# Kernel optimization log

Hardware: AMD Instinct MI355X
Metric: run time of the kernel (lower is better)

## Reference

```python
import math
import jax, jax.numpy as jnp
import numpy as np

B, S, D, H, FF, E, V, RH = 8, 256, 512, 8, 2048, 8, 32000, 256
MAX_PATH, MAX_VISITS = 4, 2
NEG = -1e9
DH = D // H


def _make_pe():
    # PositionalEncoding buffer (sin/cos), sliced to seq len S
    pos = np.arange(S, dtype=np.float32)[:, None]
    div = np.exp(np.arange(0, D, 2, dtype=np.float32) * (-math.log(10000.0) / D))
    pe = np.zeros((S, D), dtype=np.float32)
    pe[:, 0::2] = np.sin(pos * div)
    pe[:, 1::2] = np.cos(pos * div)
    return jnp.asarray(pe[None])  # [1,S,D]


def setup_inputs() -> dict:
    key = jax.random.key(0)
    ks = jax.random.split(key, 12)
    s = 0.02
    return dict(
        input_ids=jax.random.randint(ks[0], (B, S), 0, V),
        emb=jax.random.normal(ks[1], (V, D), jnp.float32) * s,
        pe=_make_pe(),
        Wqkv=jax.random.normal(ks[2], (E, 3 * D, D), jnp.float32) * s,
        bqkv=jnp.zeros((E, 3 * D), jnp.float32),
        Wo=jax.random.normal(ks[3], (E, D, D), jnp.float32) * s,
        bo=jnp.zeros((E, D), jnp.float32),
        W1=jax.random.normal(ks[4], (E, FF, D), jnp.float32) * s,
        b1=jnp.zeros((E, FF), jnp.float32),
        W2=jax.random.normal(ks[5], (E, D, FF), jnp.float32) * s,
        b2=jnp.zeros((E, D), jnp.float32),
        ln1_g=jnp.ones((E, D), jnp.float32), ln1_b=jnp.zeros((E, D), jnp.float32),
        ln2_g=jnp.ones((E, D), jnp.float32), ln2_b=jnp.zeros((E, D), jnp.float32),
        tag=jax.random.normal(ks[6], (E, D), jnp.float32) * 0.01,
        r_w1=jax.random.normal(ks[7], (RH, D), jnp.float32) * s,
        r_b1=jnp.zeros((RH,), jnp.float32),
        r_w2=jax.random.normal(ks[8], (E + 1, RH), jnp.float32) * s,
        r_b2=jnp.zeros((E + 1,), jnp.float32),
        lm_w=jax.random.normal(ks[9], (V, D), jnp.float32) * s,
        lm_b=jnp.zeros((V,), jnp.float32),
    )


def _ln(x, g, b):
    # per-sample gathered LayerNorm params g,b: [B,D]; x: [B,S,D]
    mu = x.mean(-1, keepdims=True)
    var = ((x - mu) ** 2).mean(-1, keepdims=True)
    return (x - mu) * jax.lax.rsqrt(var + 1e-5) * g[:, None, :] + b[:, None, :]


def _expert(x, idx, Wqkv, bqkv, Wo, bo, W1, b1, W2, b2, g1, be1, g2, be2, tag):
    # post-norm TransformerEncoderLayer (eval mode, dropout off) with per-sample expert params
    qkv = jnp.einsum('bsd,bfd->bsf', x, Wqkv[idx]) + bqkv[idx][:, None, :]
    q, k, v = jnp.split(qkv, 3, axis=-1)
    q = q.reshape(B, S, H, DH)
    k = k.reshape(B, S, H, DH)
    v = v.reshape(B, S, H, DH)
    att = jax.nn.softmax(jnp.einsum('bqhd,bkhd->bhqk', q, k) / math.sqrt(DH), axis=-1)
    ctx = jnp.einsum('bhqk,bkhd->bqhd', att, v).reshape(B, S, D)
    attn_out = jnp.einsum('bsd,bod->bso', ctx, Wo[idx]) + bo[idx][:, None, :]
    x = _ln(x + attn_out, g1[idx], be1[idx])
    hid = jax.nn.relu(jnp.einsum('bsd,bfd->bsf', x, W1[idx]) + b1[idx][:, None, :])
    ff = jnp.einsum('bsf,bdf->bsd', hid, W2[idx]) + b2[idx][:, None, :]
    x = _ln(x + ff, g2[idx], be2[idx])
    return x + tag[idx][:, None, :]  # + specialization_tag


def reference(input_ids, emb, pe, Wqkv, bqkv, Wo, bo, W1, b1, W2, b2,
              ln1_g, ln1_b, ln2_g, ln2_b, tag, r_w1, r_b1, r_w2, r_b2, lm_w, lm_b):
    pad_mask = (jnp.arange(V) != 0).astype(emb.dtype)[:, None]  # padding_idx=0 row is zero
    rep = (emb * pad_mask)[input_ids] * math.sqrt(D) + pe[:, :S]
    visits = jnp.zeros((B, E), jnp.int32)
    active = jnp.ones((B,), bool)
    ent_total = jnp.asarray(0.0, rep.dtype)
    for _ in range(MAX_PATH):
        summary = rep.mean(1)  # [B,D]
        h = jax.nn.relu(summary @ r_w1.T + r_b1)
        logits = h @ r_w2.T + r_b2  # [B,E+1], last slot = terminate
        logits = jnp.concatenate(
            [jnp.where(visits >= MAX_VISITS, NEG, logits[:, :E]), logits[:, E:]], axis=1)
        probs = jax.nn.softmax(logits, axis=-1)
        ent = -jnp.sum(probs * jnp.log(probs + 1e-9), axis=-1)
        cnt = jnp.sum(active)
        ent_total = ent_total + jnp.where(
            cnt > 0, jnp.sum(ent * active) / jnp.maximum(cnt, 1).astype(ent.dtype), 0.0)
        choice = jnp.argmax(logits, axis=-1)       # eval mode: hard argmax
        go = active & (choice < E)                 # samples routed to an expert this step
        idx = jnp.where(go, choice, 0)
        visits = visits + jax.nn.one_hot(idx, E, dtype=jnp.int32) * go[:, None].astype(jnp.int32)
        new_rep = _expert(rep, idx, Wqkv, bqkv, Wo, bo, W1, b1, W2, b2,
                          ln1_g, ln1_b, ln2_g, ln2_b, tag)
        rep = jnp.where(go[:, None, None], new_rep, rep)  # terminated/inactive reps frozen
        active = go
    logits_lm = rep @ lm_w.T + lm_b  # [B,S,V]
    return logits_lm, ent_total
```

## Files before the change

kernel.cpp:

```cpp
#include <hip/hip_runtime.h>
#include <hip/hip_bf16.h>

#define NB 8
#define NS 256
#define ND 512
#define NH 8
#define NDH 64
#define NFF 2048
#define NE 8
#define NV 32000
#define NRH 256
#define MAXV 2
#define NEGV (-1e9f)

typedef __attribute__((ext_vector_type(8))) short short8;
typedef __attribute__((ext_vector_type(4))) float f32x4;

__device__ __forceinline__ unsigned short f2bf(float x) {
  unsigned int u = __float_as_uint(x);
  u = (u + 0x7fffu + ((u >> 16) & 1u)) >> 16;
  return (unsigned short)u;
}

__device__ __forceinline__ void gload16(const unsigned short* g, unsigned short* l) {
  __builtin_amdgcn_global_load_lds(
      (const __attribute__((address_space(1))) unsigned int*)g,
      (__attribute__((address_space(3))) unsigned int*)l, 16, 0, 0);
}

__device__ __forceinline__ int swzc(int lane) {
  return (lane & 3) ^ ((lane >> 3) & 3);
}

__device__ __forceinline__ void cast8(const float* s, unsigned short* d, int j) {
  const float4* s4 = (const float4*)s;
  float4 a = s4[j * 2], b = s4[j * 2 + 1];
  short8 v;
  v[0] = (short)f2bf(a.x); v[1] = (short)f2bf(a.y);
  v[2] = (short)f2bf(a.z); v[3] = (short)f2bf(a.w);
  v[4] = (short)f2bf(b.x); v[5] = (short)f2bf(b.y);
  v[6] = (short)f2bf(b.z); v[7] = (short)f2bf(b.w);
  *(short8*)&d[(size_t)j * 8] = v;
}

__global__ __launch_bounds__(256) void k_cast5e(
    const float* s0, unsigned short* d0, int n0,
    const float* s1, unsigned short* d1, int n1,
    const float* s2, unsigned short* d2, int n2,
    const float* s3, unsigned short* d3, int n3,
    const float* s4, unsigned short* d4, int n4,
    int nbcast,
    const int* __restrict__ ids, const float* __restrict__ emb,
    const float* __restrict__ pe, float* __restrict__ rep,
    unsigned short* __restrict__ repb, float* __restrict__ partial,
    int* visits, int* active, float* entp) {
  if (blockIdx.x == 0) {
    if (threadIdx.x < NB * NE) visits[threadIdx.x] = 0;
    if (threadIdx.x < NB) active[threadIdx.x] = 1;
    if (threadIdx.x == 0) *entp = 0.f;
  }
  if ((int)blockIdx.x >= nbcast) {
    int j2 = blockIdx.x - nbcast;
    int rg = j2 & 15, b = j2 >> 4;
    int t = threadIdx.x;
    int c0 = t, c1 = t + 256;
    float p0 = 0.f, p1 = 0.f;
    for (int row = 0; row < 16; ++row) {
      int s = rg * 16 + row;
      int id = ids[b * NS + s];
      float sc = (id != 0) ? 22.627416997969522f : 0.f;
      float v0 = emb[(size_t)id * ND + c0] * sc + pe[(size_t)s * ND + c0];
      float v1 = emb[(size_t)id * ND + c1] * sc + pe[(size_t)s * ND + c1];
      size_t base = ((size_t)b * NS + s) * ND;
      rep[base + c0] = v0; rep[base + c1] = v1;
      repb[base + c0] = f2bf(v0); repb[base + c1] = f2bf(v1);
      p0 += v0; p1 += v1;
    }
    float* pp = partial + ((size_t)b * 16 + rg) * ND;
    pp[c0] = p0; pp[c1] = p1;
    return;
  }
  int j = blockIdx.x * 256 + threadIdx.x;
  if (j < n0) { cast8(s0, d0, j); return; }
  j -= n0;
  if (j < n1) { cast8(s1, d1, j); return; }
  j -= n1;
  if (j < n2) { cast8(s2, d2, j); return; }
  j -= n2;
  if (j < n3) { cast8(s3, d3, j); return; }
  j -= n3;
  if (j < n4) cast8(s4, d4, j);
}

__global__ __launch_bounds__(256) void k_router(const float* __restrict__ partial,
                                                const float* __restrict__ rw1,
                                                const float* __restrict__ rb1,
                                                const float* __restrict__ rw2,
                                                const float* __restrict__ rb2,
                                                int* visits, int* active,
                                                int* idx, int* go, float* ent_total) {
  __shared__ float sm[NB][ND];
  __shared__ float h[NB][NRH];
  __shared__ float lg[NB][NE + 1];
  int t = threadIdx.x;
  for (int i = t; i < NB * ND; i += 256) {
    int bb = i >> 9, d = i & 511;
    const float* pp = partial + ((size_t)bb * 16) * ND + d;
    float s = 0.f;
#pragma unroll
    for (int rg = 0; rg < 16; ++rg) s += pp[(size_t)rg * ND];
    sm[bb][d] = s * (1.f / NS);
  }
  __syncthreads();
  {
    const float* w = rw1 + (size_t)t * ND;
    float acc[NB];
#pragma unroll
    for (int b = 0; b < NB; ++b) acc[b] = rb1[t];
    for (int d = 0; d < ND; ++d) {
      float wv = w[d];
#pragma unroll
      for (int b = 0; b < NB; ++b) acc[b] += sm[b][d] * wv;
    }
#pragma unroll
    for (int b = 0; b < NB; ++b) h[b][t] = fmaxf(acc[b], 0.f);
  }
  __syncthreads();
  if (t < NB * (NE + 1)) {
    int b = t / (NE + 1), e = t % (NE + 1);
    const float* w = rw2 + e * NRH;
    float a = rb2[e];
    for (int r = 0; r < NRH; ++r) a += h[b][r] * w[r];
    lg[b][e] = a;
  }
  __syncthreads();
  if (t == 0) {
    int aprev[NB];
    int cnt = 0;
    for (int b = 0; b < NB; ++b) { aprev[b] = active[b]; cnt += aprev[b]; }
    float entsum = 0.f;
    for (int b = 0; b < NB; ++b) {
      float l[NE + 1];
      for (int e = 0; e < NE; ++e)
        l[e] = (visits[b * NE + e] >= MAXV) ? NEGV : lg[b][e];
      l[NE] = lg[b][NE];
      float m = l[0];
      for (int e = 1; e <= NE; ++e) m = fmaxf(m, l[e]);
      float z = 0.f, p[NE + 1];
      for (int e = 0; e <= NE; ++e) { p[e] = __expf(l[e] - m); z += p[e]; }
      float zi = 1.f / z, ent = 0.f;
      for (int e = 0; e <= NE; ++e) {
        float pp = p[e] * zi;
        ent -= pp * __logf(pp + 1e-9f);
      }
      if (aprev[b]) entsum += ent;
      int ch = 0; float bm = l[0];
      for (int e = 1; e <= NE; ++e) if (l[e] > bm) { bm = l[e]; ch = e; }
      int g = (aprev[b] && ch < NE) ? 1 : 0;
      int ix = g ? ch : 0;
      visits[b * NE + ix] += g;
      idx[b] = ix; go[b] = g; active[b] = g;
    }
    if (cnt > 0) *ent_total += entsum / (float)cnt;
  }
}

template <int OUT, int RELU, int SK>
__global__ __launch_bounds__(256) void k_gemm64p(
    const unsigned short* __restrict__ Aall, int sa,
    const unsigned short* __restrict__ Wall, const float* __restrict__ ball,
    float* __restrict__ Pall, unsigned short* __restrict__ Uall, int so,
    int N, int K,
    unsigned short* __restrict__ Qb, unsigned short* __restrict__ Kb,
    unsigned short* __restrict__ Vt,
    const int* __restrict__ go, const int* __restrict__ idx) {
  int b = blockIdx.z;
  if (!go[b]) return;
  int t = threadIdx.x;
  int lane = t & 63, w = t >> 6;
  int wm = (w >> 1) * 32, wn = (w & 1) * 32;
  int kc = blockIdx.x >> 2;
  int bm = (blockIdx.x & 3) * 64, bn = blockIdx.y * 64;
  int KC = K / SK;
  int lrow = (lane >> 4) * 4, lcol = lane & 15;
  const unsigned short* A = Aall + (size_t)b * sa + kc * KC;
  const unsigned short* W = Wall + (size_t)idx[b] * N * K + kc * KC;

  __shared__ __align__(16) unsigned short As[3][64][32];
  __shared__ __align__(16) unsigned short Bs[3][64][32];
  f32x4 acc[2][2];
#pragma unroll
  for (int i = 0; i < 2; ++i)
#pragma unroll
    for (int j = 0; j < 2; ++j) acc[i][j] = (f32x4){0.f, 0.f, 0.f, 0.f};

  const unsigned short* ga = A + (size_t)(bm + w * 16 + (lane >> 2)) * K + swzc(lane) * 8;
  const unsigned short* gb = W + (size_t)(bn + w * 16 + (lane >> 2)) * K + swzc(lane) * 8;

#define ISSUE64(slot, kt)                        \
  gload16(ga + (kt) * 32, &As[slot][w * 16][0]); \
  gload16(gb + (kt) * 32, &Bs[slot][w * 16][0]);

  int nk = KC >> 5;
  ISSUE64(0, 0)
  ISSUE64(1, 1)
  ISSUE64(2, 2)

  int row0 = lane & 15;
  int cs = ((lane >> 4) ^ ((row0 >> 1) & 3)) * 8;
  for (int it = 0; it < nk; ++it) {
    int rem = nk - 1 - it;
    if (rem >= 2)      asm volatile("s_waitcnt vmcnt(4)" ::: "memory");
    else if (rem == 1) asm volatile("s_waitcnt vmcnt(2)" ::: "memory");
    else               asm volatile("s_waitcnt vmcnt(0)" ::: "memory");
    asm volatile("s_barrier" ::: "memory");
    int sl = it % 3;
    short8 a[2], bfr[2];
#pragma unroll
    for (int mf = 0; mf < 2; ++mf)
      a[mf] = *(const short8*)&As[sl][wm + mf * 16 + row0][cs];
#pragma unroll
    for (int nf = 0; nf < 2; ++nf)
      bfr[nf] = *(const short8*)&Bs[sl][wn + nf * 16 + row0][cs];
#pragma unroll
    for (int mf = 0; mf < 2; ++mf)
#pragma unroll
      for (int nf = 0; nf < 2; ++nf)
        acc[mf][nf] = __builtin_amdgcn_mfma_f32_16x16x32_bf16(a[mf], bfr[nf], acc[mf][nf], 0, 0, 0);
    asm volatile("s_barrier" ::: "memory");
    if (it + 3 < nk) { ISSUE64(sl, it + 3) }
  }
#undef ISSUE64

  if (OUT == 2) {
    const float* bias = ball + (size_t)idx[b] * N;
    int seg = bn >> 9;
#pragma unroll
    for (int nf = 0; nf < 2; ++nf) {
      int col = bn + wn + nf * 16 + lcol;
      float bv = bias[col];
      if (seg < 2) {
        unsigned short* dst = (seg == 0) ? Qb : Kb;
        int cc = col - seg * 512;
#pragma unroll
        for (int mf = 0; mf < 2; ++mf)
#pragma unroll
          for (int r = 0; r < 4; ++r) {
            int row = bm + wm + mf * 16 + lrow + r;
            dst[((size_t)b * NS + row) * ND + cc] = f2bf(acc[mf][nf][r] + bv);
          }
      } else {
        int dcol = col - 1024;
#pragma unroll
        for (int mf = 0; mf < 2; ++mf) {
          int s0 = bm + wm + mf * 16 + lrow;
          unsigned long long pk =
              (unsigned long long)f2bf(acc[mf][nf][0] + bv) |
              ((unsigned long long)f2bf(acc[mf][nf][1] + bv) << 16) |
              ((unsigned long long)f2bf(acc[mf][nf][2] + bv) << 32) |
              ((unsigned long long)f2bf(acc[mf][nf][3] + bv) << 48);
          *(unsigned long long*)&Vt[((size_t)b * 512 + dcol) * 256 + s0] = pk;
        }
      }
    }
  } else if (OUT == 1) {
    const float* bias = ball + (size_t)idx[b] * N;
#pragma unroll
    for (int nf = 0; nf < 2; ++nf) {
      int col = bn + wn + nf * 16 + lcol;
      float bv = bias[col];
#pragma unroll
      for (int mf = 0; mf < 2; ++mf) {
#pragma unroll
        for (int r = 0; r < 4; ++r) {
          int row = bm + wm + mf * 16 + lrow + r;
          float v = acc[mf][nf][r] + bv;
          if (RELU) v = fmaxf(v, 0.f);
          Uall[(size_t)b * so + (size_t)row * N + col] = f2bf(v);
        }
      }
    }
  } else {
    float* P = Pall + ((size_t)kc * NB + b) * ((size_t)NS * N);
#pragma unroll
    for (int nf = 0; nf < 2; ++nf) {
      int col = bn + wn + nf * 16 + lcol;
#pragma unroll
      for (int mf = 0; mf < 2; ++mf)
#pragma unroll
        for (int r = 0; r < 4; ++r)
          P[(size_t)(bm + wm + mf * 16 + lrow + r) * N + col] = acc[mf][nf][r];
    }
  }
}

__global__ __launch_bounds__(256) void k_attn2(const unsigned short* __restrict__ Qb,
                                               const unsigned short* __restrict__ Kb,
                                               const unsigned short* __restrict__ Vt,
                                               unsigned short* __restrict__ ctxb,
                                               const int* __restrict__ go) {
  int b = blockIdx.z, h = blockIdx.y, qt = blockIdx.x;
  if (!go[b]) return;
  int t = threadIdx.x;
  __shared__ __align__(16) unsigned short lds0[16384];
  __shared__ __align__(16) unsigned short lds1[16384];
  int lane = t & 63, w = t >> 6, g = lane >> 4, c = lane & 15;

#pragma unroll
  for (int i = 0; i < 8; ++i) {
    int task = i * 256 + t;
    int k = task >> 3, cc = task & 7;
    short8 v = *(const short8*)&Kb[((size_t)b * NS + k) * ND + h * NDH + cc * 8];
    *(short8*)&lds0[k * 64 + ((cc * 8) ^ ((k & 7) << 3))] = v;
  }
#pragma unroll
  for (int i = 0; i < 8; ++i) {
    int task = i * 256 + t;
    int d = task >> 5, kc = task & 31;
    short8 v = *(const short8*)&Vt[((size_t)b * 512 + h * NDH + d) * 256 + kc * 8];
    *(short8*)&lds1[d * 256 + ((kc * 8) ^ ((d & 7) << 3))] = v;
  }
  short8 qf[2];
  {
    const unsigned short* qp = Qb + ((size_t)b * NS + qt * 64 + w * 16 + c) * ND + h * NDH;
    qf[0] = *(const short8*)&qp[g * 8];
    qf[1] = *(const short8*)&qp[32 + g * 8];
  }
  __syncthreads();

  f32x4 sacc[16];
#pragma unroll
  for (int mf = 0; mf < 16; ++mf) sacc[mf] = (f32x4){0.f, 0.f, 0.f, 0.f};
#pragma unroll
  for (int mf = 0; mf < 16; ++mf) {
#pragma unroll
    for (int kd = 0; kd < 2; ++kd) {
      int row = mf * 16 + c;
      short8 kf = *(const short8*)&lds0[row * 64 + ((kd * 32 + g * 8) ^ ((row & 7) << 3))];
      sacc[mf] = __builtin_amdgcn_mfma_f32_16x16x32_bf16(kf, qf[kd], sacc[mf], 0, 0, 0);
    }
  }
  __syncthreads();

  float mx = -3.4e38f;
#pragma unroll
  for (int mf = 0; mf < 16; ++mf) {
#pragma unroll
    for (int r = 0; r < 4; ++r) {
      sacc[mf][r] *= 0.125f;
      mx = fmaxf(mx, sacc[mf][r]);
    }
  }
  mx = fmaxf(mx, __shfl_xor(mx, 16));
  mx = fmaxf(mx, __shfl_xor(mx, 32));
  float sum = 0.f;
#pragma unroll
  for (int mf = 0; mf < 16; ++mf)
#pragma unroll
    for (int r = 0; r < 4; ++r) {
      float p = __expf(sacc[mf][r] - mx);
      sacc[mf][r] = p;
      sum += p;
    }
  sum += __shfl_xor(sum, 16);
  sum += __shfl_xor(sum, 32);
  float zi = 1.f / sum;

  int q_l = w * 16 + c;
#pragma unroll
  for (int mf = 0; mf < 16; ++mf) {
    unsigned long long pk =
        (unsigned long long)f2bf(sacc[mf][0] * zi) |
        ((unsigned long long)f2bf(sacc[mf][1] * zi) << 16) |
        ((unsigned long long)f2bf(sacc[mf][2] * zi) << 32) |
        ((unsigned long long)f2bf(sacc[mf][3] * zi) << 48);
    *(unsigned long long*)&lds0[q_l * 256 + ((mf * 16 + g * 4) ^ ((q_l & 7) << 3))] = pk;
  }

  f32x4 cacc[4];
#pragma unroll
  for (int nf = 0; nf < 4; ++nf) cacc[nf] = (f32x4){0.f, 0.f, 0.f, 0.f};
#pragma unroll
  for (int ks = 0; ks < 8; ++ks) {
    int prow = w * 16 + c;
    short8 pf = *(const short8*)&lds0[prow * 256 + ((ks * 32 + g * 8) ^ ((prow & 7) << 3))];
#pragma unroll
    for (int nf = 0; nf < 4; ++nf) {
      int vrow = nf * 16 + c;
      short8 vf = *(const short8*)&lds1[vrow * 256 + ((ks * 32 + g * 8) ^ ((vrow & 7) << 3))];
      cacc[nf] = __builtin_amdgcn_mfma_f32_16x16x32_bf16(pf, vf, cacc[nf], 0, 0, 0);
    }
  }
#pragma unroll
  for (int nf = 0; nf < 4; ++nf)
#pragma unroll
    for (int r = 0; r < 4; ++r)
      ctxb[((size_t)b * NS + qt * 64 + w * 16 + g * 4 + r) * ND + h * NDH + nf * 16 + c] =
          f2bf(cacc[nf][r]);
}

template <int NCH, int TAG, int SUMP>
__global__ __launch_bounds__(256) void k_ln_red(
    const float* __restrict__ res, const float* __restrict__ part,
    const float* __restrict__ gbias,
    const float* __restrict__ gall, const float* __restrict__ beall,
    const float* __restrict__ tagall,
    float* __restrict__ outf, unsigned short* __restrict__ outb,
    float* __restrict__ sump,
    const int* __restrict__ go, const int* __restrict__ idx) {
  int b = blockIdx.y;
  if (!go[b]) return;
  int rg = blockIdx.x;
  int w = threadIdx.x >> 6, l = threadIdx.x & 63;
  int ix = idx[b];
  int d = l * 8;
  float gb8[8], gg[8], bb[8];
  {
    float4 a0 = *(const float4*)&gbias[ix * ND + d];
    float4 a1 = *(const float4*)&gbias[ix * ND + d + 4];
    gb8[0] = a0.x; gb8[1] = a0.y; gb8[2] = a0.z; gb8[3] = a0.w;
    gb8[4] = a1.x; gb8[5] = a1.y; gb8[6] = a1.z; gb8[7] = a1.w;
    float4 g0 = *(const float4*)&gall[ix * ND + d];
    float4 g1 = *(const float4*)&gall[ix * ND + d + 4];
    gg[0] = g0.x; gg[1] = g0.y; gg[2] = g0.z; gg[3] = g0.w;
    gg[4] = g1.x; gg[5] = g1.y; gg[6] = g1.z; gg[7] = g1.w;
    float4 b0 = *(const float4*)&beall[ix * ND + d];
    float4 b1 = *(const float4*)&beall[ix * ND + d + 4];
    bb[0] = b0.x; bb[1] = b0.y; bb[2] = b0.z; bb[3] = b0.w;
    bb[4] = b1.x; bb[5] = b1.y; bb[6] = b1.z; bb[7] = b1.w;
    if (TAG) {
      float4 t0 = *(const float4*)&tagall[ix * ND + d];
      float4 t1 = *(const float4*)&tagall[ix * ND + d + 4];
      bb[0] += t0.x; bb[1] += t0.y; bb[2] += t0.z; bb[3] += t0.w;
      bb[4] += t1.x; bb[5] += t1.y; bb[6] += t1.z; bb[7] += t1.w;
    }
  }
  float ps[8] = {0.f, 0.f, 0.f, 0.f, 0.f, 0.f, 0.f, 0.f};
  const size_t CSTRIDE = (size_t)NB * NS * ND;
  for (int rr = 0; rr < 4; ++rr) {
    int s = rg * 16 + w * 4 + rr;
    size_t base = ((size_t)b * NS + s) * ND;
    float4 x0 = *(const float4*)&res[base + d];
    float4 x1 = *(const float4*)&res[base + d + 4];
    float v[8] = {x0.x + gb8[0], x0.y + gb8[1], x0.z + gb8[2], x0.w + gb8[3],
                  x1.x + gb8[4], x1.y + gb8[5], x1.z + gb8[6], x1.w + gb8[7]};
#pragma unroll
    for (int c = 0; c < NCH; ++c) {
      const float* pc = part + c * CSTRIDE + base;
      float4 p0 = *(const float4*)&pc[d];
      float4 p1 = *(const float4*)&pc[d + 4];
      v[0] += p0.x; v[1] += p0.y; v[2] += p0.z; v[3] += p0.w;
      v[4] += p1.x; v[5] += p1.y; v[6] += p1.z; v[7] += p1.w;
    }
    float sum = 0.f;
#pragma unroll
    for (int j = 0; j < 8; ++j) sum += v[j];
#pragma unroll
    for (int off = 1; off < 64; off <<= 1) sum += __shfl_xor(sum, off);
    float mu = sum * (1.f / ND);
    float var = 0.f;
#pragma unroll
    for (int j = 0; j < 8; ++j) { v[j] -= mu; var += v[j] * v[j]; }
#pragma unroll
    for (int off = 1; off < 64; off <<= 1) var += __shfl_xor(var, off);
    float rs = rsqrtf(var * (1.f / ND) + 1e-5f);
    float o[8];
    short8 ob;
#pragma unroll
    for (int j = 0; j < 8; ++j) {
      o[j] = v[j] * rs * gg[j] + bb[j];
      if (SUMP) ps[j] += o[j];
      ob[j] = (short)f2bf(o[j]);
    }
    *(float4*)&outf[base + d] = (float4){o[0], o[1], o[2], o[3]};
    *(float4*)&outf[base + d + 4] = (float4){o[4], o[5], o[6], o[7]};
    *(short8*)&outb[base + d] = ob;
  }
  if (SUMP) {
    __shared__ float pl[4][ND];
#pragma unroll
    for (int j = 0; j < 8; ++j) pl[w][d + j] = ps[j];
    __syncthreads();
    if (w == 0) {
      float* pp = sump + ((size_t)b * 16 + rg) * ND;
#pragma unroll
      for (int j = 0; j < 8; ++j)
        pp[d + j] = pl[0][d + j] + pl[1][d + j] + pl[2][d + j] + pl[3][d + j];
    }
  }
}

__global__ __launch_bounds__(512, 2) void k_lmhead256(const unsigned short* __restrict__ Ab,
                                                      const unsigned short* __restrict__ Wb,
                                                      const float* __restrict__ bias,
                                                      float* __restrict__ out,
                                                      const float* __restrict__ entp) {
  if (blockIdx.x == 0 && threadIdx.x == 0)
    out[(size_t)NB * NS * NV] = *entp;
  int id = blockIdx.x;
  int swz = (id & 7) * 125 + (id >> 3);
  int bm = (swz % 8) * 256;
  int bn = (swz / 8) * 256;

  __shared__ __align__(16) unsigned short As[2][256][32];
  __shared__ __align__(16) unsigned short Bs[2][256][32];
  int t = threadIdx.x;
  int lane = t & 63, w = t >> 6;
  int wm = (w >> 2) * 128, wn = (w & 3) * 64;
  f32x4 acc[8][4];
#pragma unroll
  for (int i = 0; i < 8; ++i)
#pragma unroll
    for (int j = 0; j < 4; ++j) acc[i][j] = (f32x4){0.f, 0.f, 0.f, 0.f};

  const unsigned short* ga = Ab + (size_t)(bm + w * 32 + (lane >> 2)) * ND + swzc(lane) * 8;
  const unsigned short* gb = Wb + (size_t)(bn + w * 32 + (lane >> 2)) * ND + swzc(lane) * 8;

#define ISSUEL(slot, kt)                                           \
  gload16(ga + (kt) * 32, &As[slot][w * 32][0]);                   \
  gload16(ga + (kt) * 32 + 16 * ND, &As[slot][w * 32 + 16][0]);    \
  gload16(gb + (kt) * 32, &Bs[slot][w * 32][0]);                   \
  gload16(gb + (kt) * 32 + 16 * ND, &Bs[slot][w * 32 + 16][0]);

  ISSUEL(0, 0)
  ISSUEL(1, 1)

  int row0 = lane & 15;
  int cs = ((lane >> 4) ^ ((row0 >> 1) & 3)) * 8;
  for (int it = 0; it < 16; ++it) {
    if (it < 15) asm volatile("s_waitcnt vmcnt(4)" ::: "memory");
    else         asm volatile("s_waitcnt vmcnt(0)" ::: "memory");
    asm volatile("s_barrier" ::: "memory");
    int sl = it & 1;
    short8 a[8], bfr[4];
#pragma unroll
    for (int mf = 0; mf < 8; ++mf)
      a[mf] = *(const short8*)&As[sl][wm + mf * 16 + row0][cs];
#pragma unroll
    for (int nf = 0; nf < 4; ++nf)
      bfr[nf] = *(const short8*)&Bs[sl][wn + nf * 16 + row0][cs];
#pragma unroll
    for (int mf = 0; mf < 8; ++mf)
#pragma unroll
      for (int nf = 0; nf < 4; ++nf)
        acc[mf][nf] = __builtin_amdgcn_mfma_f32_16x16x32_bf16(a[mf], bfr[nf], acc[mf][nf], 0, 0, 0);
    asm volatile("s_barrier" ::: "memory");
    if (it + 2 < 16) { ISSUEL(sl, it + 2) }
  }
#undef ISSUEL

  int lrow = (lane >> 4) * 4, lcol = lane & 15;
#pragma unroll
  for (int nf = 0; nf < 4; ++nf) {
    int col = bn + wn + nf * 16 + lcol;
    float bv = bias[col];
#pragma unroll
    for (int mf = 0; mf < 8; ++mf) {
#pragma unroll
      for (int r = 0; r < 4; ++r) {
        int row = bm + wm + mf * 16 + lrow + r;
        out[(size_t)row * NV + col] = acc[mf][nf][r] + bv;
      }
    }
  }
}

extern "C" void kernel_launch(void* const* d_in, const int* in_sizes, int n_in,
                              void* d_out, int out_size, void* d_ws, size_t ws_size,
                              hipStream_t stream) {
  const int* ids   = (const int*)d_in[0];
  const float* emb = (const float*)d_in[1];
  const float* pe  = (const float*)d_in[2];
  const float* Wqkv = (const float*)d_in[3];
  const float* bqkv = (const float*)d_in[4];
  const float* Wo   = (const float*)d_in[5];
  const float* bo   = (const float*)d_in[6];
  const float* W1   = (const float*)d_in[7];
  const float* b1   = (const float*)d_in[8];
  const float* W2   = (const float*)d_in[9];
  const float* b2   = (const float*)d_in[10];
  const float* g1   = (const float*)d_in[11];
  const float* be1  = (const float*)d_in[12];
  const float* g2   = (const float*)d_in[13];
  const float* be2  = (const float*)d_in[14];
  const float* tag  = (const float*)d_in[15];
  const float* rw1  = (const float*)d_in[16];
  const float* rb1  = (const float*)d_in[17];
  const float* rw2  = (const float*)d_in[18];
  const float* rb2  = (const float*)d_in[19];
  const float* lmw  = (const float*)d_in[20];
  const float* lmb  = (const float*)d_in[21];
  float* out = (float*)d_out;

  float* ws = (float*)d_ws;
  size_t o = 0;
  float* rep = ws + o;  o += (size_t)NB * NS * ND;
  float* x1  = ws + o;  o += (size_t)NB * NS * ND;
  float* partk = ws + o; o += (size_t)4 * NB * NS * ND;
  float* partial = ws + o; o += (size_t)NB * 16 * ND;
  int* visits = (int*)(ws + o); o += 1024;
  int* active = visits + NB * NE;
  int* idx = active + NB;
  int* go = idx + NB;
  float* entp = (float*)(go + NB);

  unsigned short* us = (unsigned short*)(ws + o);
  size_t uo = 0;
  unsigned short* rep_b = us + uo; uo += (size_t)NB * NS * ND;
  unsigned short* x1_b  = us + uo; uo += (size_t)NB * NS * ND;
  unsigned short* ctx_b = us + uo; uo += (size_t)NB * NS * ND;
  unsigned short* Qb    = us + uo; uo += (size_t)NB * NS * ND;
  unsigned short* Kb    = us + uo; uo += (size_t)NB * NS * ND;
  unsigned short* Vt    = us + uo; uo += (size_t)NB * NS * ND;
  unsigned short* hid_b = us + uo; uo += (size_t)NB * NS * NFF;
  unsigned short* Wqkv_b = us + uo; uo += (size_t)NE * 3 * ND * ND;
  unsigned short* Wo_b   = us + uo; uo += (size_t)NE * ND * ND;
  unsigned short* W1_b   = us + uo; uo += (size_t)NE * NFF * ND;
  unsigned short* W2_b   = us + uo; uo += (size_t)NE * ND * NFF;
  unsigned short* lmw_b  = us + uo; uo += (size_t)NV * ND;

  {
    int n0 = NE * 3 * ND * ND / 8, n1 = NE * ND * ND / 8, n2 = NE * NFF * ND / 8,
        n3 = NE * ND * NFF / 8, n4 = NV * ND / 8;
    int nbcast = (n0 + n1 + n2 + n3 + n4) / 256;
    k_cast5e<<<nbcast + 16 * NB, 256, 0, stream>>>(
        Wqkv, Wqkv_b, n0, Wo, Wo_b, n1, W1, W1_b, n2, W2, W2_b, n3, lmw, lmw_b, n4,
        nbcast, ids, emb, pe, rep, rep_b, partial, visits, active, entp);
  }

  for (int step = 0; step < 4; ++step) {
    k_router<<<1, 256, 0, stream>>>(partial, rw1, rb1, rw2, rb2,
                                    visits, active, idx, go, entp);
    k_gemm64p<2, 0, 1><<<dim3(4, 24, NB), 256, 0, stream>>>(
        rep_b, NS * ND, Wqkv_b, bqkv, nullptr, nullptr, 0, 3 * ND, ND,
        Qb, Kb, Vt, go, idx);
    k_attn2<<<dim3(4, NH, NB), 256, 0, stream>>>(Qb, Kb, Vt, ctx_b, go);
    k_gemm64p<0, 0, 2><<<dim3(8, 8, NB), 256, 0, stream>>>(
        ctx_b, NS * ND, Wo_b, nullptr, partk, nullptr, 0, ND, ND,
        nullptr, nullptr, nullptr, go, idx);
    k_ln_red<2, 0, 0><<<dim3(16, NB), 256, 0, stream>>>(
        rep, partk, bo, g1, be1, nullptr, x1, x1_b, nullptr, go, idx);
    k_gemm64p<1, 1, 1><<<dim3(4, 32, NB), 256, 0, stream>>>(
        x1_b, NS * ND, W1_b, b1, nullptr, hid_b, NS * NFF, NFF, ND,
        nullptr, nullptr, nullptr, go, idx);
    k_gemm64p<0, 0, 4><<<dim3(16, 8, NB), 256, 0, stream>>>(
        hid_b, NS * NFF, W2_b, nullptr, partk, nullptr, 0, ND, NFF,
        nullptr, nullptr, nullptr, go, idx);
    k_ln_red<4, 1, 1><<<dim3(16, NB), 256, 0, stream>>>(
        x1, partk, b2, g2, be2, tag, rep, rep_b, partial, go, idx);
  }

  k_lmhead256<<<1000, 512, 0, stream>>>(rep_b, lmw_b, lmb, out, entp);
}
```

Baseline: 587.8 us.

## Use 64-wide K tiles with double buffering and read attention K/V directly from global

```diff
diff --git a/kernel.cpp b/kernel.cpp
--- a/kernel.cpp
+++ b/kernel.cpp
@@ -186,49 +186,48 @@
   const unsigned short* A = Aall + (size_t)b * sa + kc * KC;
   const unsigned short* W = Wall + (size_t)idx[b] * N * K + kc * KC;
 
-  __shared__ __align__(16) unsigned short As[3][64][32];
-  __shared__ __align__(16) unsigned short Bs[3][64][32];
+  __shared__ __align__(16) unsigned short As[2][64][64];
+  __shared__ __align__(16) unsigned short Bs[2][64][64];
   f32x4 acc[2][2];
 #pragma unroll
   for (int i = 0; i < 2; ++i)
 #pragma unroll
     for (int j = 0; j < 2; ++j) acc[i][j] = (f32x4){0.f, 0.f, 0.f, 0.f};
 
-  const unsigned short* ga = A + (size_t)(bm + w * 16 + (lane >> 2)) * K + swzc(lane) * 8;
-  const unsigned short* gb = W + (size_t)(bn + w * 16 + (lane >> 2)) * K + swzc(lane) * 8;
-
-#define ISSUE64(slot, kt)                        \
-  gload16(ga + (kt) * 32, &As[slot][w * 16][0]); \
-  gload16(gb + (kt) * 32, &Bs[slot][w * 16][0]);
-
-  int nk = KC >> 5;
+  int ch8 = (lane & 7) ^ ((lane >> 3) & 7);
+  const unsigned short* ga = A + (size_t)(bm + w * 16 + (lane >> 3)) * K + ch8 * 8;
+  const unsigned short* gb = W + (size_t)(bn + w * 16 + (lane >> 3)) * K + ch8 * 8;
+
+#define ISSUE64(slot, kt)                                            \
+  gload16(ga + (size_t)(kt) * 64, &As[slot][w * 16][0]);             \
+  gload16(ga + (size_t)(kt) * 64 + 8 * (size_t)K, &As[slot][w * 16 + 8][0]); \
+  gload16(gb + (size_t)(kt) * 64, &Bs[slot][w * 16][0]);             \
+  gload16(gb + (size_t)(kt) * 64 + 8 * (size_t)K, &Bs[slot][w * 16 + 8][0]);
+
+  int nk = KC >> 6;
   ISSUE64(0, 0)
   ISSUE64(1, 1)
-  ISSUE64(2, 2)
-
-  int row0 = lane & 15;
-  int cs = ((lane >> 4) ^ ((row0 >> 1) & 3)) * 8;
+
+  int row0 = lane & 15, g = lane >> 4;
   for (int it = 0; it < nk; ++it) {
-    int rem = nk - 1 - it;
-    if (rem >= 2)      asm volatile("s_waitcnt vmcnt(4)" ::: "memory");
-    else if (rem == 1) asm volatile("s_waitcnt vmcnt(2)" ::: "memory");
-    else               asm volatile("s_waitcnt vmcnt(0)" ::: "memory");
+    if (it < nk - 1) asm volatile("s_waitcnt vmcnt(4)" ::: "memory");
+    else             asm volatile("s_waitcnt vmcnt(0)" ::: "memory");
     asm volatile("s_barrier" ::: "memory");
-    int sl = it % 3;
-    short8 a[2], bfr[2];
-#pragma unroll
-    for (int mf = 0; mf < 2; ++mf)
-      a[mf] = *(const short8*)&As[sl][wm + mf * 16 + row0][cs];
-#pragma unroll
-    for (int nf = 0; nf < 2; ++nf)
-      bfr[nf] = *(const short8*)&Bs[sl][wn + nf * 16 + row0][cs];
-#pragma unroll
-    for (int mf = 0; mf < 2; ++mf)
-#pragma unroll
-      for (int nf = 0; nf < 2; ++nf)
-        acc[mf][nf] = __builtin_amdgcn_mfma_f32_16x16x32_bf16(a[mf], bfr[nf], acc[mf][nf], 0, 0, 0);
+    int sl = it & 1;
+#pragma unroll
+    for (int kk = 0; kk < 2; ++kk) {
+      int co = ((kk * 4 + g) ^ (row0 & 7)) * 8;
+      short8 a0 = *(const short8*)&As[sl][wm + row0][co];
+      short8 a1 = *(const short8*)&As[sl][wm + 16 + row0][co];
+      short8 b0 = *(const short8*)&Bs[sl][wn + row0][co];
+      short8 b1 = *(const short8*)&Bs[sl][wn + 16 + row0][co];
+      acc[0][0] = __builtin_amdgcn_mfma_f32_16x16x32_bf16(a0, b0, acc[0][0], 0, 0, 0);
+      acc[0][1] = __builtin_amdgcn_mfma_f32_16x16x32_bf16(a0, b1, acc[0][1], 0, 0, 0);
+      acc[1][0] = __builtin_amdgcn_mfma_f32_16x16x32_bf16(a1, b0, acc[1][0], 0, 0, 0);
+      acc[1][1] = __builtin_amdgcn_mfma_f32_16x16x32_bf16(a1, b1, acc[1][1], 0, 0, 0);
+    }
     asm volatile("s_barrier" ::: "memory");
-    if (it + 3 < nk) { ISSUE64(sl, it + 3) }
+    if (it + 2 < nk) { ISSUE64(sl, it + 2) }
   }
 #undef ISSUE64
 
@@ -302,45 +301,29 @@
   int b = blockIdx.z, h = blockIdx.y, qt = blockIdx.x;
   if (!go[b]) return;
   int t = threadIdx.x;
-  __shared__ __align__(16) unsigned short lds0[16384];
-  __shared__ __align__(16) unsigned short lds1[16384];
+  __shared__ __align__(16) unsigned short ldsP[16384];
   int lane = t & 63, w = t >> 6, g = lane >> 4, c = lane & 15;
 
-#pragma unroll
-  for (int i = 0; i < 8; ++i) {
-    int task = i * 256 + t;
-    int k = task >> 3, cc = task & 7;
-    short8 v = *(const short8*)&Kb[((size_t)b * NS + k) * ND + h * NDH + cc * 8];
-    *(short8*)&lds0[k * 64 + ((cc * 8) ^ ((k & 7) << 3))] = v;
-  }
-#pragma unroll
-  for (int i = 0; i < 8; ++i) {
-    int task = i * 256 + t;
-    int d = task >> 5, kc = task & 31;
-    short8 v = *(const short8*)&Vt[((size_t)b * 512 + h * NDH + d) * 256 + kc * 8];
-    *(short8*)&lds1[d * 256 + ((kc * 8) ^ ((d & 7) << 3))] = v;
-  }
   short8 qf[2];
   {
     const unsigned short* qp = Qb + ((size_t)b * NS + qt * 64 + w * 16 + c) * ND + h * NDH;
     qf[0] = *(const short8*)&qp[g * 8];
     qf[1] = *(const short8*)&qp[32 + g * 8];
   }
-  __syncthreads();
-
+
+  const unsigned short* kbase = Kb + ((size_t)b * NS) * ND + h * NDH;
   f32x4 sacc[16];
 #pragma unroll
   for (int mf = 0; mf < 16; ++mf) sacc[mf] = (f32x4){0.f, 0.f, 0.f, 0.f};
 #pragma unroll
   for (int mf = 0; mf < 16; ++mf) {
+    int row = mf * 16 + c;
 #pragma unroll
     for (int kd = 0; kd < 2; ++kd) {
-      int row = mf * 16 + c;
-      short8 kf = *(const short8*)&lds0[row * 64 + ((kd * 32 + g * 8) ^ ((row & 7) << 3))];
+      short8 kf = *(const short8*)&kbase[(size_t)row * ND + kd * 32 + g * 8];
       sacc[mf] = __builtin_amdgcn_mfma_f32_16x16x32_bf16(kf, qf[kd], sacc[mf], 0, 0, 0);
     }
   }
-  __syncthreads();
 
   float mx = -3.4e38f;
 #pragma unroll
@@ -374,20 +357,21 @@
         ((unsigned long long)f2bf(sacc[mf][1] * zi) << 16) |
         ((unsigned long long)f2bf(sacc[mf][2] * zi) << 32) |
         ((unsigned long long)f2bf(sacc[mf][3] * zi) << 48);
-    *(unsigned long long*)&lds0[q_l * 256 + ((mf * 16 + g * 4) ^ ((q_l & 7) << 3))] = pk;
-  }
+    *(unsigned long long*)&ldsP[q_l * 256 + ((mf * 16 + g * 4) ^ ((q_l & 7) << 3))] = pk;
+  }
+  __syncthreads();
 
   f32x4 cacc[4];
 #pragma unroll
   for (int nf = 0; nf < 4; ++nf) cacc[nf] = (f32x4){0.f, 0.f, 0.f, 0.f};
+  const unsigned short* vbase = Vt + ((size_t)b * 512 + h * NDH) * 256;
 #pragma unroll
   for (int ks = 0; ks < 8; ++ks) {
     int prow = w * 16 + c;
-    short8 pf = *(const short8*)&lds0[prow * 256 + ((ks * 32 + g * 8) ^ ((prow & 7) << 3))];
+    short8 pf = *(const short8*)&ldsP[prow * 256 + ((ks * 32 + g * 8) ^ ((prow & 7) << 3))];
 #pragma unroll
     for (int nf = 0; nf < 4; ++nf) {
-      int vrow = nf * 16 + c;
-      short8 vf = *(const short8*)&lds1[vrow * 256 + ((ks * 32 + g * 8) ^ ((vrow & 7) << 3))];
+      short8 vf = *(const short8*)&vbase[(size_t)(nf * 16 + c) * 256 + ks * 32 + g * 8];
       cacc[nf] = __builtin_amdgcn_mfma_f32_16x16x32_bf16(pf, vf, cacc[nf], 0, 0, 0);
     }
   }
```

New measurement: 595.4 us. No clear change (+1.3%).
